# Kernel optimization log

Measured on AMD Instinct MI355X. Metric: run time of the kernel, lower is better.

The kernel has to match this reference:

```python
import jax, jax.numpy as jnp
import numpy as np

BS, S, E, H = 64, 512, 1024, 16
HD = E // H
MASK_ID, KNOW_ID = 30001, 30002


def setup_inputs() -> dict:
    key = jax.random.key(0)
    ks = jax.random.split(key, 8)
    model_output = jax.random.normal(ks[0], (BS, S, E), dtype=jnp.float32)
    ids = jax.random.randint(ks[1], (BS, S), 0, 30000)  # never hits special ids
    ids = ids.at[:, 0].set(MASK_ID)        # exactly one [MASK] per sequence
    ids = ids.at[:, 1:9].set(KNOW_ID)      # 8 knowledge slots per sequence
    knowledge_output = jax.random.normal(ks[2], (BS, E), dtype=jnp.float32)
    empty_knowledge_mask = jax.random.randint(ks[3], (BS,), 0, 2).astype(bool)
    bound = 1.0 / np.sqrt(E)
    in_proj_weight = jax.random.uniform(ks[4], (3 * E, E), minval=-bound, maxval=bound, dtype=jnp.float32)
    in_proj_bias = jnp.zeros((3 * E,), jnp.float32)
    out_proj_weight = jax.random.uniform(ks[5], (E, E), minval=-bound, maxval=bound, dtype=jnp.float32)
    out_proj_bias = jnp.zeros((E,), jnp.float32)
    attention_strength = jnp.float32(0.1)
    return {
        "model_output": model_output,
        "knowledge_output": knowledge_output,
        "in_proj_weight": in_proj_weight,
        "in_proj_bias": in_proj_bias,
        "out_proj_weight": out_proj_weight,
        "out_proj_bias": out_proj_bias,
        "attention_strength": attention_strength,
        "input_ids": ids,
        "empty_knowledge_mask": empty_knowledge_mask,
        "knowledge_token_id": KNOW_ID,
        "mask_token_id": MASK_ID,
    }


def reference(model_output, knowledge_output, in_proj_weight, in_proj_bias,
              out_proj_weight, out_proj_bias, attention_strength,
              input_ids, empty_knowledge_mask, knowledge_token_id, mask_token_id):
    bs, sent_len, hidden = model_output.shape
    # --- knowledge injection: scatter knowledge vector into knowledge-token slots ---
    knowledge_mask = input_ids == knowledge_token_id                 # [bs, S]
    kv_src = jnp.where(knowledge_mask[:, :, None],
                       knowledge_output[:, None, :], model_output)  # [bs, S, E]
    # --- single-query gather: one [MASK] position per sequence ---
    mask_pos = jnp.argmax(input_ids == mask_token_id, axis=1)        # [bs]
    q_in = jnp.take_along_axis(kv_src, mask_pos[:, None, None], axis=1)[:, 0, :]  # [bs, E]
    # --- nn.MultiheadAttention (eval mode, dropout=0) ---
    Wq, Wk, Wv = in_proj_weight[:E], in_proj_weight[E:2 * E], in_proj_weight[2 * E:]
    bq, bk, bv = in_proj_bias[:E], in_proj_bias[E:2 * E], in_proj_bias[2 * E:]
    q = (q_in @ Wq.T + bq).reshape(bs, H, HD)                        # [bs, H, hd]
    k = (kv_src @ Wk.T + bk).reshape(bs, sent_len, H, HD)            # [bs, S, H, hd]
    v = (kv_src @ Wv.T + bv).reshape(bs, sent_len, H, HD)
    scale = 1.0 / np.sqrt(HD)
    scores = jnp.einsum('bhd,bshd->bhs', q * scale, k)               # [bs, H, S]
    attn = jax.nn.softmax(scores, axis=-1)
    ctx = jnp.einsum('bhs,bshd->bhd', attn, v).reshape(bs, hidden)   # [bs, E]
    attn_output = ctx @ out_proj_weight.T + out_proj_bias            # [bs, E]
    # --- residual on the ORIGINAL (pre-injection) mask-token states ---
    origin_q = jnp.take_along_axis(model_output, mask_pos[:, None, None], axis=1)[:, 0, :]
    mask_output = origin_q + attention_strength * attn_output
    # --- conditional restore where knowledge is empty ---
    mask_output = jnp.where(empty_knowledge_mask[:, None], origin_q, mask_output)
    return mask_output
```

## Files before the change

kernel.cpp:

```cpp
#include <hip/hip_runtime.h>

#define BS 64
#define S  512
#define E  1024
#define H  16
#define HD 64
#define SCALE 0.125f
#define CATT 8

#define W_QIN  1024
#define W_QKBF 66560
#define W_NUM  1115136
#define W_DEN  9503744
#define W_CTX  9511936

typedef __attribute__((ext_vector_type(8))) short short8;
typedef __attribute__((ext_vector_type(4))) float floatx4;

union S8u { uint2 u2[2]; short8 s; };

__device__ __forceinline__ unsigned short bf16c(float x) {
    unsigned int u = __float_as_uint(x);
    return (unsigned short)((u + 0x7fffu + ((u >> 16) & 1u)) >> 16);
}
__device__ __forceinline__ unsigned int pack_bf16(float a, float b) {
    return (unsigned int)bf16c(a) | ((unsigned int)bf16c(b) << 16);
}
__device__ __forceinline__ void fma4(float4& acc, float s, const float4& v) {
    acc.x += s * v.x; acc.y += s * v.y; acc.z += s * v.z; acc.w += s * v.w;
}
__device__ __forceinline__ float dot4(const float4& a, const float4& b) {
    return a.x * b.x + a.y * b.y + a.z * b.z + a.w * b.w;
}
__device__ __forceinline__ void bfly8(float* a) {
    #pragma unroll
    for (int off = 32; off > 0; off >>= 1) {
        #pragma unroll
        for (int i = 0; i < 8; i++) a[i] += __shfl_xor(a[i], off, 64);
    }
}

__global__ void k_prep(const float* __restrict__ model, const float* __restrict__ knowledge,
                       const int* __restrict__ ids, const int* __restrict__ mask_id_p,
                       const int* __restrict__ kid_p, int* __restrict__ mp,
                       float* __restrict__ qin) {
    int b = blockIdx.x, tid = threadIdx.x;
    __shared__ int best;
    if (tid == 0) best = S;
    __syncthreads();
    int mid = mask_id_p[0];
    for (int s = tid; s < S; s += 256)
        if (ids[b * S + s] == mid) atomicMin(&best, s);
    __syncthreads();
    int m = (best == S) ? 0 : best;
    if (tid == 0) mp[b] = m;
    bool isk = (ids[b * S + m] == kid_p[0]);
    const float* qrow = isk ? knowledge + (size_t)b * E : model + ((size_t)(b * S + m)) * E;
    ((float4*)(qin + (size_t)b * E))[tid] = ((const float4*)qrow)[tid];
}

__global__ void k_qgen(const float* __restrict__ qin, const float* __restrict__ w_in,
                       const float* __restrict__ b_in, unsigned short* __restrict__ qkbf) {
    int h = blockIdx.x, b0 = blockIdx.y * 4, t = threadIdx.x;
    __shared__ float qin_l[4][1024];
    __shared__ float qred[4][64][4];
    __shared__ float qs_l[4][64];
    #pragma unroll
    for (int k = 0; k < 4; k++) {
        int idx4 = k * 256 + t;
        int bb = idx4 >> 8, col = (idx4 & 255) * 4;
        *(float4*)&qin_l[bb][col] = *(const float4*)(qin + (size_t)(b0 + bb) * E + col);
    }
    __syncthreads();
    {
        int d = t >> 2, part = t & 3;
        const float* wr = w_in + (size_t)(h * HD + d) * E + part * 256;
        float acc[4] = {0.f, 0.f, 0.f, 0.f};
        #pragma unroll 8
        for (int i = 0; i < 64; i++) {
            float4 wv = *(const float4*)(wr + i * 4);
            #pragma unroll
            for (int bb = 0; bb < 4; bb++)
                acc[bb] += dot4(wv, *(const float4*)&qin_l[bb][part * 256 + i * 4]);
        }
        #pragma unroll
        for (int bb = 0; bb < 4; bb++) qred[bb][d][part] = acc[bb];
    }
    __syncthreads();
    if (t < 64) {
        float bias = b_in[h * HD + t];
        #pragma unroll
        for (int bb = 0; bb < 4; bb++)
            qs_l[bb][t] = qred[bb][t][0] + qred[bb][t][1] + qred[bb][t][2] + qred[bb][t][3] + bias;
    }
    __syncthreads();
    {
        int e0 = t * 4;
        const float* wk = w_in + (size_t)(E + h * HD) * E + e0;
        float4 acc[4];
        #pragma unroll
        for (int bb = 0; bb < 4; bb++) acc[bb] = make_float4(0.f, 0.f, 0.f, 0.f);
        #pragma unroll 8
        for (int d = 0; d < HD; d++) {
            float4 wv = *(const float4*)(wk + (size_t)d * E);
            #pragma unroll
            for (int bb = 0; bb < 4; bb++) fma4(acc[bb], qs_l[bb][d], wv);
        }
        #pragma unroll
        for (int bb = 0; bb < 4; bb++) {
            uint2 pk;
            pk.x = pack_bf16(acc[bb].x * SCALE, acc[bb].y * SCALE);
            pk.y = pack_bf16(acc[bb].z * SCALE, acc[bb].w * SCALE);
            *(uint2*)&qkbf[((size_t)(b0 + bb) * H + h) * E + e0] = pk;
        }
    }
}

__global__ __launch_bounds__(512, 4) void k_attn(
    const float* __restrict__ model, const float* __restrict__ knowledge,
    const int* __restrict__ ids, const int* __restrict__ kid_p,
    const unsigned short* __restrict__ qkbf, float* __restrict__ num, float* __restrict__ den) {
    __shared__ __align__(16) unsigned char Ubuf[73984];
    unsigned short* Rbuf  = (unsigned short*)Ubuf;
    unsigned short* RbufT = (unsigned short*)(Ubuf + 33024);
    float* Tbuf = (float*)Ubuf;
    __shared__ unsigned short Pbuf[16 * 40];
    __shared__ float Sred[4][16][17];
    __shared__ unsigned long long kmask_s;

    int tid = threadIdx.x;
    int w = tid >> 6, l = tid & 63;
    int quad = l >> 4, lm = l & 15;
    int b = blockIdx.x, c = blockIdx.y;
    int s0 = c * 64;

    if (w == 0) {
        int id = ids[b * S + s0 + l];
        unsigned long long mk = __ballot(id == kid_p[0]);
        if (l == 0) kmask_s = mk;
    }
    floatx4 accn[8];
    #pragma unroll
    for (int i = 0; i < 8; i++) accn[i] = (floatx4)0.f;
    float accden = 0.f;
    const float* kb = knowledge + (size_t)b * E;
    const float* mb = model + (size_t)b * S * E;
    short8 qfr[8];
    if (w < 4) {
        const unsigned short* qh = qkbf + ((size_t)b * H + lm) * E;
        #pragma unroll
        for (int t = 0; t < 8; t++)
            qfr[t] = *(const short8*)(const void*)(qh + (w * 8 + t) * 32 + quad * 8);
    }
    __syncthreads();
    unsigned long long kmask = kmask_s;

    int hi = tid >> 8;
    int col4 = (tid & 255) * 4;
    const float* base0 = mb + (size_t)(s0 + hi) * E + col4;
    const float* kbase = kb + col4;

    float4 pf[8];
    #pragma unroll
    for (int k = 0; k < 8; k++) {
        int s = k * 2 + hi;
        const float* rp = ((kmask >> s) & 1ull) ? kbase : base0 + (size_t)(k * 2) * E;
        pf[k] = *(const float4*)rp;
    }

    for (int pass = 0; pass < 4; pass++) {
        #pragma unroll
        for (int k = 0; k < 8; k++) {
            int row = k * 2 + hi;
            float4 v = pf[k];
            unsigned short h0 = bf16c(v.x), h1 = bf16c(v.y), h2 = bf16c(v.z), h3 = bf16c(v.w);
            uint2 pk;
            pk.x = (unsigned int)h0 | ((unsigned int)h1 << 16);
            pk.y = (unsigned int)h2 | ((unsigned int)h3 << 16);
            *(uint2*)&Rbuf[row * 1032 + col4] = pk;
            RbufT[(col4 + 0) * 20 + row] = h0;
            RbufT[(col4 + 1) * 20 + row] = h1;
            RbufT[(col4 + 2) * 20 + row] = h2;
            RbufT[(col4 + 3) * 20 + row] = h3;
        }
        __syncthreads();
        if (pass < 3) {
            int rb = (pass + 1) * 16;
            #pragma unroll
            for (int k = 0; k < 8; k++) {
                int s = rb + k * 2 + hi;
                const float* rp = ((kmask >> s) & 1ull) ? kbase : base0 + (size_t)(rb + k * 2) * E;
                pf[k] = *(const float4*)rp;
            }
        }
        if (w < 4) {
            floatx4 acs = (floatx4)0.f;
            #pragma unroll
            for (int t = 0; t < 8; t++) {
                int kk = w * 8 + t;
                short8 a = *(const short8*)(const void*)&Rbuf[lm * 1032 + kk * 32 + quad * 8];
                acs = __builtin_amdgcn_mfma_f32_16x16x32_bf16(a, qfr[t], acs, 0, 0, 0);
            }
            Sred[w][quad * 4 + 0][lm] = acs[0];
            Sred[w][quad * 4 + 1][lm] = acs[1];
            Sred[w][quad * 4 + 2][lm] = acs[2];
            Sred[w][quad * 4 + 3][lm] = acs[3];
        }
        __syncthreads();
        if (w == 0) {
            float ex[4];
            #pragma unroll
            for (int r = 0; r < 4; r++) {
                int row = quad * 4 + r;
                float s = Sred[0][row][lm] + Sred[1][row][lm] + Sred[2][row][lm] + Sred[3][row][lm];
                ex[r] = __expf(s);
                accden += ex[r];
            }
            uint2 pw;
            pw.x = (unsigned int)bf16c(ex[0]) | ((unsigned int)bf16c(ex[1]) << 16);
            pw.y = (unsigned int)bf16c(ex[2]) | ((unsigned int)bf16c(ex[3]) << 16);
            *(uint2*)&Pbuf[lm * 40 + quad * 4] = pw;
        }
        __syncthreads();
        short8 afr = {};
        if (quad < 2) afr = *(const short8*)(const void*)&Pbuf[lm * 40 + quad * 8];
        #pragma unroll
        for (int i = 0; i < 8; i++) {
            int e = (w * 8 + i) * 16 + lm;
            S8u bb; bb.s = (short8){};
            if (quad < 2) {
                bb.u2[0] = *(const uint2*)&RbufT[e * 20 + quad * 8];
                bb.u2[1] = *(const uint2*)&RbufT[e * 20 + quad * 8 + 4];
            }
            accn[i] = __builtin_amdgcn_mfma_f32_16x16x32_bf16(afr, bb.s, accn[i], 0, 0, 0);
        }
        __syncthreads();
    }
    #pragma unroll
    for (int i = 0; i < 8; i++) {
        int e = (w * 8 + i) * 16 + lm;
        Tbuf[(quad * 4 + 0) * 1028 + e] = accn[i][0];
        Tbuf[(quad * 4 + 1) * 1028 + e] = accn[i][1];
        Tbuf[(quad * 4 + 2) * 1028 + e] = accn[i][2];
        Tbuf[(quad * 4 + 3) * 1028 + e] = accn[i][3];
    }
    if (w == 0) {
        accden += __shfl_xor(accden, 16, 64);
        accden += __shfl_xor(accden, 32, 64);
        if (l < 16) den[(size_t)(c * BS + b) * H + l] = accden;
    }
    __syncthreads();
    size_t base = ((size_t)(c * BS + b) * H) * E;
    #pragma unroll
    for (int k = 0; k < 8; k++) {
        int idx4 = k * 512 + tid;
        int h = idx4 >> 8, e4 = (idx4 & 255) * 4;
        *(float4*)(num + base + (size_t)idx4 * 4) = *(const float4*)&Tbuf[h * 1028 + e4];
    }
}

__global__ void k_pc(const float* __restrict__ num, const float* __restrict__ den,
                     const float* __restrict__ w_in, const float* __restrict__ b_in,
                     float* __restrict__ ctx) {
    int h = blockIdx.x, b0 = blockIdx.y * 4, t = threadIdx.x;
    __shared__ float p_l[4][1024];
    __shared__ float cred[4][64][4];
    __shared__ float inv_l[4];
    #pragma unroll
    for (int k = 0; k < 4; k++) {
        int idx4 = k * 256 + t;
        int bb = idx4 >> 8, e4 = (idx4 & 255) * 4;
        float4 a = make_float4(0.f, 0.f, 0.f, 0.f);
        #pragma unroll
        for (int cc = 0; cc < CATT; cc++) {
            float4 v = *(const float4*)(num + (((size_t)(cc * BS + b0 + bb) * H + h) * E) + e4);
            a.x += v.x; a.y += v.y; a.z += v.z; a.w += v.w;
        }
        *(float4*)&p_l[bb][e4] = a;
    }
    if (t < 4) {
        float ds = 0.f;
        for (int cc = 0; cc < CATT; cc++) ds += den[(size_t)(cc * BS + b0 + t) * H + h];
        inv_l[t] = 1.0f / ds;
    }
    __syncthreads();
    {
        int jj = t >> 2, part = t & 3;
        const float* wr = w_in + (size_t)(2 * E + h * HD + jj) * E + part * 256;
        float acc[4] = {0.f, 0.f, 0.f, 0.f};
        #pragma unroll 8
        for (int i = 0; i < 64; i++) {
            float4 wv = *(const float4*)(wr + i * 4);
            #pragma unroll
            for (int bb = 0; bb < 4; bb++)
                acc[bb] += dot4(wv, *(const float4*)&p_l[bb][part * 256 + i * 4]);
        }
        #pragma unroll
        for (int bb = 0; bb < 4; bb++) cred[bb][jj][part] = acc[bb];
    }
    __syncthreads();
    if (t < 64) {
        float bias = b_in[2 * E + h * HD + t];
        #pragma unroll
        for (int bb = 0; bb < 4; bb++) {
            float s = cred[bb][t][0] + cred[bb][t][1] + cred[bb][t][2] + cred[bb][t][3];
            ctx[(size_t)(b0 + bb) * E + h * HD + t] = inv_l[bb] * s + bias;
        }
    }
}

__global__ void k_out(const float* __restrict__ model, const float* __restrict__ w_out,
                      const float* __restrict__ b_out, const float* __restrict__ ctx,
                      const int* __restrict__ mp, const int* __restrict__ empty,
                      const float* __restrict__ strength_p, float* __restrict__ out) {
    int w = threadIdx.x >> 6, l = threadIdx.x & 63;
    int j = blockIdx.x * 4 + w;
    int b0 = blockIdx.y * 8;
    const float* wr = w_out + (size_t)j * E;
    float4 wv[4];
    #pragma unroll
    for (int r = 0; r < 4; r++) wv[r] = *(const float4*)(wr + r * 256 + l * 4);
    float acc[8];
    #pragma unroll
    for (int bb = 0; bb < 8; bb++) {
        const float* src = ctx + (size_t)(b0 + bb) * E;
        float a = 0.f;
        #pragma unroll
        for (int r = 0; r < 4; r++) a += dot4(wv[r], *(const float4*)(src + r * 256 + l * 4));
        acc[bb] = a;
    }
    bfly8(acc);
    if (l < 8) {
        float myacc = acc[0];
        #pragma unroll
        for (int bb = 1; bb < 8; bb++) myacc = (l == bb) ? acc[bb] : myacc;
        int b = b0 + l;
        int m = mp[b];
        float orig = model[((size_t)(b * S + m)) * E + j];
        float bias = b_out[j];
        float st = strength_p[0];
        out[(size_t)b * E + j] = empty[b] ? orig : orig + st * (myacc + bias);
    }
}

extern "C" void kernel_launch(void* const* d_in, const int* in_sizes, int n_in,
                              void* d_out, int out_size, void* d_ws, size_t ws_size,
                              hipStream_t stream) {
    const float* model     = (const float*)d_in[0];
    const float* knowledge = (const float*)d_in[1];
    const float* w_in      = (const float*)d_in[2];
    const float* b_in      = (const float*)d_in[3];
    const float* w_out     = (const float*)d_in[4];
    const float* b_out     = (const float*)d_in[5];
    const float* strength  = (const float*)d_in[6];
    const int*   ids       = (const int*)d_in[7];
    const int*   empty     = (const int*)d_in[8];
    const int*   know_id   = (const int*)d_in[9];
    const int*   mask_id   = (const int*)d_in[10];
    float* out = (float*)d_out;

    float* ws  = (float*)d_ws;
    int*   mp  = (int*)d_ws;
    float* qin = ws + W_QIN;
    unsigned short* qkbf = (unsigned short*)(ws + W_QKBF);
    float* num = ws + W_NUM;
    float* den = ws + W_DEN;
    float* ctx = ws + W_CTX;

    k_prep<<<BS, 256, 0, stream>>>(model, knowledge, ids, mask_id, know_id, mp, qin);
    k_qgen<<<dim3(H, 16), 256, 0, stream>>>(qin, w_in, b_in, qkbf);
    k_attn<<<dim3(BS, CATT), 512, 0, stream>>>(model, knowledge, ids, know_id, qkbf, num, den);
    k_pc<<<dim3(H, 16), 256, 0, stream>>>(num, den, w_in, b_in, ctx);
    k_out<<<dim3(256, 8), 256, 0, stream>>>(model, w_out, b_out, ctx, mp, empty, strength, out);
}
```

Baseline: 292.7 us.

## Compute softmax exps in registers per wave, drop P buffer barrier, swap grid order

Each wave now computes the exponentials of the score tile directly into its own MFMA A-fragment, instead of wave 0 writing bf16 probabilities to shared memory. This removes the Pbuf buffer and one block-wide barrier per pass. The query fragments are reloaded from global memory (through cache) inside the loop rather than held in registers, which frees VGPRs but adds a load per MFMA. The grid is also transposed so that blocks working on the same batch are adjacent in launch order, which may improve cache locality for the knowledge and q rows.

```diff
diff --git a/kernel.cpp b/kernel.cpp
--- a/kernel.cpp
+++ b/kernel.cpp
@@ -124,14 +124,13 @@
     unsigned short* Rbuf  = (unsigned short*)Ubuf;
     unsigned short* RbufT = (unsigned short*)(Ubuf + 33024);
     float* Tbuf = (float*)Ubuf;
-    __shared__ unsigned short Pbuf[16 * 40];
     __shared__ float Sred[4][16][17];
     __shared__ unsigned long long kmask_s;
 
     int tid = threadIdx.x;
     int w = tid >> 6, l = tid & 63;
     int quad = l >> 4, lm = l & 15;
-    int b = blockIdx.x, c = blockIdx.y;
+    int c = blockIdx.x, b = blockIdx.y;
     int s0 = c * 64;
 
     if (w == 0) {
@@ -145,13 +144,7 @@
     float accden = 0.f;
     const float* kb = knowledge + (size_t)b * E;
     const float* mb = model + (size_t)b * S * E;
-    short8 qfr[8];
-    if (w < 4) {
-        const unsigned short* qh = qkbf + ((size_t)b * H + lm) * E;
-        #pragma unroll
-        for (int t = 0; t < 8; t++)
-            qfr[t] = *(const short8*)(const void*)(qh + (w * 8 + t) * 32 + quad * 8);
-    }
+    const unsigned short* qh = qkbf + ((size_t)b * H + lm) * E;
     __syncthreads();
     unsigned long long kmask = kmask_s;
 
@@ -198,8 +191,9 @@
             #pragma unroll
             for (int t = 0; t < 8; t++) {
                 int kk = w * 8 + t;
-                short8 a = *(const short8*)(const void*)&Rbuf[lm * 1032 + kk * 32 + quad * 8];
-                acs = __builtin_amdgcn_mfma_f32_16x16x32_bf16(a, qfr[t], acs, 0, 0, 0);
+                short8 a  = *(const short8*)(const void*)&Rbuf[lm * 1032 + kk * 32 + quad * 8];
+                short8 bf = *(const short8*)(const void*)(qh + kk * 32 + quad * 8);
+                acs = __builtin_amdgcn_mfma_f32_16x16x32_bf16(a, bf, acs, 0, 0, 0);
             }
             Sred[w][quad * 4 + 0][lm] = acs[0];
             Sred[w][quad * 4 + 1][lm] = acs[1];
@@ -207,23 +201,21 @@
             Sred[w][quad * 4 + 3][lm] = acs[3];
         }
         __syncthreads();
-        if (w == 0) {
-            float ex[4];
-            #pragma unroll
-            for (int r = 0; r < 4; r++) {
-                int row = quad * 4 + r;
-                float s = Sred[0][row][lm] + Sred[1][row][lm] + Sred[2][row][lm] + Sred[3][row][lm];
-                ex[r] = __expf(s);
-                accden += ex[r];
+        S8u afr; afr.s = (short8){};
+        if (quad < 2) {
+            float ex[8];
+            #pragma unroll
+            for (int j = 0; j < 8; j++) {
+                int row = quad * 8 + j;
+                float sc = Sred[0][row][lm] + Sred[1][row][lm] + Sred[2][row][lm] + Sred[3][row][lm];
+                ex[j] = __expf(sc);
             }
-            uint2 pw;
-            pw.x = (unsigned int)bf16c(ex[0]) | ((unsigned int)bf16c(ex[1]) << 16);
-            pw.y = (unsigned int)bf16c(ex[2]) | ((unsigned int)bf16c(ex[3]) << 16);
-            *(uint2*)&Pbuf[lm * 40 + quad * 4] = pw;
-        }
-        __syncthreads();
-        short8 afr = {};
-        if (quad < 2) afr = *(const short8*)(const void*)&Pbuf[lm * 40 + quad * 8];
+            accden += ex[0] + ex[1] + ex[2] + ex[3] + ex[4] + ex[5] + ex[6] + ex[7];
+            afr.u2[0].x = pack_bf16(ex[0], ex[1]);
+            afr.u2[0].y = pack_bf16(ex[2], ex[3]);
+            afr.u2[1].x = pack_bf16(ex[4], ex[5]);
+            afr.u2[1].y = pack_bf16(ex[6], ex[7]);
+        }
         #pragma unroll
         for (int i = 0; i < 8; i++) {
             int e = (w * 8 + i) * 16 + lm;
@@ -232,7 +224,7 @@
                 bb.u2[0] = *(const uint2*)&RbufT[e * 20 + quad * 8];
                 bb.u2[1] = *(const uint2*)&RbufT[e * 20 + quad * 8 + 4];
             }
-            accn[i] = __builtin_amdgcn_mfma_f32_16x16x32_bf16(afr, bb.s, accn[i], 0, 0, 0);
+            accn[i] = __builtin_amdgcn_mfma_f32_16x16x32_bf16(afr.s, bb.s, accn[i], 0, 0, 0);
         }
         __syncthreads();
     }
@@ -246,7 +238,6 @@
     }
     if (w == 0) {
         accden += __shfl_xor(accden, 16, 64);
-        accden += __shfl_xor(accden, 32, 64);
         if (l < 16) den[(size_t)(c * BS + b) * H + l] = accden;
     }
     __syncthreads();
@@ -369,7 +360,7 @@
 
     k_prep<<<BS, 256, 0, stream>>>(model, knowledge, ids, mask_id, know_id, mp, qin);
     k_qgen<<<dim3(H, 16), 256, 0, stream>>>(qin, w_in, b_in, qkbf);
-    k_attn<<<dim3(BS, CATT), 512, 0, stream>>>(model, knowledge, ids, know_id, qkbf, num, den);
+    k_attn<<<dim3(CATT, BS), 512, 0, stream>>>(model, knowledge, ids, know_id, qkbf, num, den);
     k_pc<<<dim3(H, 16), 256, 0, stream>>>(num, den, w_in, b_in, ctx);
     k_out<<<dim3(256, 8), 256, 0, stream>>>(model, w_out, b_out, ctx, mp, empty, strength, out);
 }
```

Result: no change. 290.0 us (-0.9%).
